# Optimization experiments

Measured on AMD Instinct MI355X. Metric: run time of the kernel, lower is better.

## Reference

```python
import jax, jax.numpy as jnp
import numpy as np

INPUT_DIM = 1024
EMBED_DIM = 1024
NUM_HEADS = 16
HEAD_DIM = EMBED_DIM // NUM_HEADS


def _xavier_uniform(key, shape):
    fan_in, fan_out = shape[1], shape[0]
    limit = float(np.sqrt(6.0 / (fan_in + fan_out)))
    return jax.random.uniform(key, shape, jnp.float32, -limit, limit)


def setup_inputs() -> dict:
    key = jax.random.key(0)
    kx, kqkv, ko = jax.random.split(key, 3)
    return {
        "x": jax.random.normal(kx, (2, 2048, INPUT_DIM), jnp.float32),
        "qkv_w": _xavier_uniform(kqkv, (3 * EMBED_DIM, INPUT_DIM)),
        "qkv_b": jnp.zeros((3 * EMBED_DIM,), jnp.float32),
        "o_w": _xavier_uniform(ko, (EMBED_DIM, INPUT_DIM)),
        "o_b": jnp.zeros((EMBED_DIM,), jnp.float32),
    }


def reference(x, qkv_w, qkv_b, o_w, o_b):
    B, S, _ = x.shape
    scale = HEAD_DIM ** -0.5
    # fused QKV projection: [B,S,3E]
    qkv = jnp.einsum('bsd,ed->bse', x, qkv_w) + qkv_b
    # [B,S,H,3Dh] -> [B,H,S,3Dh], then split into q,k,v
    qkv = qkv.reshape(B, S, NUM_HEADS, 3 * HEAD_DIM).transpose(0, 2, 1, 3)
    q, k, v = jnp.split(qkv, 3, axis=-1)
    # scaled dot-product attention
    scores = jnp.einsum('bhqd,bhkd->bhqk', q, k) * scale
    attn = jax.nn.softmax(scores, axis=-1)
    values = jnp.einsum('bhqk,bhkd->bhqd', attn, v)
    # [B,H,S,Dh] -> [B,S,E]
    values = values.transpose(0, 2, 1, 3).reshape(B, S, EMBED_DIM)
    return jnp.einsum('bse,oe->bso', values, o_w) + o_b
```

## Files before the change

### kernel.cpp

```cpp
#include <hip/hip_runtime.h>
#include <hip/hip_bf16.h>

typedef __bf16  bf16x8 __attribute__((ext_vector_type(8)));
typedef __bf16  bf16x4 __attribute__((ext_vector_type(4)));
typedef float   f32x4  __attribute__((ext_vector_type(4)));

#define LOG2E 1.44269504088896340736f

__device__ __forceinline__ void async_copy16(const void* g, void* l) {
  __builtin_amdgcn_global_load_lds(
      (const __attribute__((address_space(1))) unsigned int*)g,
      (__attribute__((address_space(3))) unsigned int*)l, 16, 0, 0);
}

#define C0 524288
#define C1 393216
#define C2 384
#define C3 131072
#define C4 128
#define CTOT (C0 + C1 + C2 + C3 + C4)
__global__ void convert_all(const void* __restrict__ x,  const void* __restrict__ qw,
                            const void* __restrict__ qb, const void* __restrict__ ow,
                            const void* __restrict__ ob,
                            __bf16* __restrict__ cx,  __bf16* __restrict__ cqw,
                            __bf16* __restrict__ cqb, __bf16* __restrict__ cow,
                            __bf16* __restrict__ cob, int* __restrict__ flag) {
  __shared__ int cnt;
  if (threadIdx.x == 0) cnt = 0;
  __syncthreads();
  unsigned int w = ((const unsigned int*)qw)[threadIdx.x];
  if (w & 0x4000u) atomicAdd(&cnt, 1);
  __syncthreads();
  const int f = (cnt > 16) ? 1 : 0;
  if (threadIdx.x == 0) *flag = f;

  int i = blockIdx.x * blockDim.x + threadIdx.x;
  const int stride = gridDim.x * blockDim.x;
  for (; i < CTOT; i += stride) {
    const void* s; __bf16* d; int off;
    if      (i < C0)                { s = x;  d = cx;  off = i; }
    else if (i < C0 + C1)           { s = qw; d = cqw; off = i - C0; }
    else if (i < C0 + C1 + C2)      { s = qb; d = cqb; off = i - C0 - C1; }
    else if (i < C0 + C1 + C2 + C3) { s = ow; d = cow; off = i - C0 - C1 - C2; }
    else                            { s = ob; d = cob; off = i - C0 - C1 - C2 - C3; }
    if (f) {
      const f32x4* sp = (const f32x4*)s;
      f32x4 a = sp[2 * off], b = sp[2 * off + 1];
      bf16x8 o;
      o[0] = (__bf16)a[0]; o[1] = (__bf16)a[1]; o[2] = (__bf16)a[2]; o[3] = (__bf16)a[3];
      o[4] = (__bf16)b[0]; o[5] = (__bf16)b[1]; o[6] = (__bf16)b[2]; o[7] = (__bf16)b[3];
      *(bf16x8*)&d[8 * off] = o;
    } else {
      *(bf16x8*)&d[8 * off] = ((const bf16x8*)s)[off];
    }
  }
}

template<int BN>
__global__ __launch_bounds__(256) void gemm_nt_bias(
    const __bf16* __restrict__ A,
    const __bf16* __restrict__ Bt,
    const __bf16* __restrict__ bias,
    __bf16* __restrict__ Cb,
    float* __restrict__ Cf,
    __bf16* __restrict__ vt,
    const int* __restrict__ flag,
    int M, int N, int K)
{
  constexpr int NI    = BN / 32;
  constexpr int BITER = (BN * 4) / 256;
  __shared__ __align__(16) __bf16 As[128 * 32];
  __shared__ __align__(16) __bf16 Bs[BN * 32];

  const int tid  = threadIdx.x;
  const int lane = tid & 63;
  const int wave = tid >> 6;
  const int qd   = lane >> 4;
  const int ln   = lane & 15;
  const int m0 = blockIdx.y * 128;
  const int n0 = blockIdx.x * BN;
  const int wm = (wave >> 1) * 64;
  const int wn = (wave & 1) * (16 * NI);

  f32x4 acc[4][NI] = {};

  for (int kt = 0; kt < K; kt += 32) {
#pragma unroll
    for (int i = 0; i < 2; ++i) {
      int s  = wave * 128 + i * 64 + lane;
      int r  = s >> 2;
      int cb = s & 3;
      async_copy16(A + (size_t)(m0 + r) * K + kt + cb * 8, &As[(wave * 128 + i * 64) * 8]);
    }
#pragma unroll
    for (int i = 0; i < BITER; ++i) {
      int s  = wave * (64 * BITER) + i * 64 + lane;
      int r  = s >> 2;
      int cb = s & 3;
      async_copy16(Bt + (size_t)(n0 + r) * K + kt + cb * 8,
                   &Bs[(wave * (64 * BITER) + i * 64) * 8]);
    }
    __syncthreads();

    bf16x8 af[4], bfr[NI];
#pragma unroll
    for (int t = 0; t < 4; ++t)
      af[t] = *(const bf16x8*)&As[(wm + t * 16 + ln) * 32 + qd * 8];
#pragma unroll
    for (int t = 0; t < NI; ++t)
      bfr[t] = *(const bf16x8*)&Bs[(wn + t * 16 + ln) * 32 + qd * 8];
#pragma unroll
    for (int mi = 0; mi < 4; ++mi)
#pragma unroll
      for (int ni = 0; ni < NI; ++ni)
        acc[mi][ni] = __builtin_amdgcn_mfma_f32_16x16x32_bf16(af[mi], bfr[ni], acc[mi][ni], 0, 0, 0);
    __syncthreads();
  }

  const bool f32out = (Cf != nullptr) && (*flag != 0);
#pragma unroll
  for (int ni = 0; ni < NI; ++ni) {
    int cb0 = n0 + wn + ni * 16;
    int col = cb0 + ln;
    float bv = (float)bias[col];
    int grp = cb0 % 192;
    if (vt != nullptr && grp >= 128) {
      int hh = cb0 / 192;
      int d  = grp - 128 + ln;
#pragma unroll
      for (int mi = 0; mi < 4; ++mi) {
        int row0 = m0 + wm + mi * 16 + qd * 4;
        int bb = row0 >> 11, ss = row0 & 2047;
        bf16x4 w;
#pragma unroll
        for (int r = 0; r < 4; ++r) w[r] = (__bf16)(acc[mi][ni][r] + bv);
        *(bf16x4*)&vt[(((size_t)(bb * 16 + hh) * 64 + d) * 2048 + ss)] = w;
      }
    } else {
#pragma unroll
      for (int mi = 0; mi < 4; ++mi) {
#pragma unroll
        for (int r = 0; r < 4; ++r) {
          int row = m0 + wm + mi * 16 + qd * 4 + r;
          float v = acc[mi][ni][r] + bv;
          if (f32out) Cf[(size_t)row * N + col] = v;
          else        Cb[(size_t)row * N + col] = (__bf16)v;
        }
      }
    }
  }
}

#define PST 72
__global__ __launch_bounds__(256, 2) void attn_flash(
    const __bf16* __restrict__ qkv,
    const __bf16* __restrict__ vt,
    __bf16* __restrict__ vals)
{
  __shared__ __align__(16) unsigned char smem[69632];
  __bf16* Ks  = (__bf16*)smem;
  __bf16* VTs = (__bf16*)(smem + 16384);
  __bf16* Ps  = (__bf16*)(smem + 32768);

  const int tid  = threadIdx.x;
  const int lane = tid & 63;
  const int wave = tid >> 6;
  const int sh   = wave >> 1;
  const int wq   = wave & 1;
  const int qd   = lane >> 4;
  const int ln   = lane & 15;
  const int b  = blockIdx.y >> 4;
  const int h  = blockIdx.y & 15;
  const int q0 = blockIdx.x * 128;
  const __bf16* base = qkv + (size_t)b * 2048 * 3072 + h * 192;
  const __bf16* vbase = vt + (size_t)(b * 16 + h) * 64 * 2048;
  const int khalf = sh * 1024;

  bf16x8 qfr[4][2];
#pragma unroll
  for (int nt = 0; nt < 4; ++nt)
#pragma unroll
    for (int ks = 0; ks < 2; ++ks)
      qfr[nt][ks] = *(const bf16x8*)&base[(size_t)(q0 + wq * 64 + nt * 16 + ln) * 3072
                                          + ks * 32 + qd * 8];

  const float kScale = 0.125f * LOG2E;
  __bf16* P = Ps + wave * (64 * PST);

  f32x4 oaccT[4][4] = {};
  float lpart[4] = {0.f, 0.f, 0.f, 0.f};

  for (int it = 0; it < 16; ++it) {
    const int kt = khalf + it * 64;
    __syncthreads();

#pragma unroll
    for (int i = 0; i < 4; ++i) {
      int s  = wq * 256 + i * 64 + lane;
      int r  = s >> 3;
      int c  = (s & 7) ^ (r & 7);
      async_copy16(base + (size_t)(kt + r) * 3072 + 64 + c * 8,
                   &Ks[sh * 4096 + (wq * 256 + i * 64) * 8]);
      async_copy16(vbase + (size_t)r * 2048 + kt + c * 8,
                   &VTs[sh * 4096 + (wq * 256 + i * 64) * 8]);
    }
    __syncthreads();

    f32x4 sacc[4][4] = {};
#pragma unroll
    for (int ks = 0; ks < 2; ++ks) {
      bf16x8 kfr[4];
#pragma unroll
      for (int mi = 0; mi < 4; ++mi) {
        int row = mi * 16 + ln;
        kfr[mi] = *(const bf16x8*)&Ks[sh * 4096 + row * 64 + (((ks * 4 + qd) ^ (row & 7)) * 8)];
      }
#pragma unroll
      for (int nt = 0; nt < 4; ++nt)
#pragma unroll
        for (int mi = 0; mi < 4; ++mi)
          sacc[nt][mi] = __builtin_amdgcn_mfma_f32_16x16x32_bf16(kfr[mi], qfr[nt][ks], sacc[nt][mi], 0, 0, 0);
    }

#pragma unroll
    for (int nt = 0; nt < 4; ++nt) {
      float rs = 0.f;
#pragma unroll
      for (int mi = 0; mi < 4; ++mi) {
        float pv[4];
#pragma unroll
        for (int r = 0; r < 4; ++r) {
          pv[r] = __builtin_exp2f(sacc[nt][mi][r] * kScale);
          rs += pv[r];
        }
        bf16x4 w;
        w[0] = (__bf16)pv[0]; w[1] = (__bf16)pv[1];
        w[2] = (__bf16)pv[2]; w[3] = (__bf16)pv[3];
        *(bf16x4*)&P[(nt * 16 + ln) * PST + mi * 16 + qd * 4] = w;
      }
      lpart[nt] += rs;
    }

    asm volatile("s_waitcnt lgkmcnt(0)" ::: "memory");

#pragma unroll
    for (int ks = 0; ks < 2; ++ks) {
      bf16x8 vfr[4], pfr[4];
#pragma unroll
      for (int md = 0; md < 4; ++md) {
        int row = md * 16 + ln;
        vfr[md] = *(const bf16x8*)&VTs[sh * 4096 + row * 64 + (((ks * 4 + qd) ^ (row & 7)) * 8)];
      }
#pragma unroll
      for (int nt = 0; nt < 4; ++nt)
        pfr[nt] = *(const bf16x8*)&P[(nt * 16 + ln) * PST + ks * 32 + qd * 8];
#pragma unroll
      for (int nt = 0; nt < 4; ++nt)
#pragma unroll
        for (int md = 0; md < 4; ++md)
          oaccT[nt][md] = __builtin_amdgcn_mfma_f32_16x16x32_bf16(vfr[md], pfr[nt], oaccT[nt][md], 0, 0, 0);
    }
  }

  float lw[4];
#pragma unroll
  for (int nt = 0; nt < 4; ++nt) {
    float l = lpart[nt];
    l += __shfl_xor(l, 16);
    l += __shfl_xor(l, 32);
    lw[nt] = l;
  }
  __syncthreads();

  float* Sc = (float*)smem;
  float* Ls = (float*)(smem + 32768);

  if (sh == 0) {
#pragma unroll
    for (int nt = 0; nt < 4; ++nt) {
#pragma unroll
      for (int md = 0; md < 4; ++md)
        *(f32x4*)&Sc[((size_t)(wq * 64 + nt * 16 + ln)) * 64 + md * 16 + qd * 4] = oaccT[nt][md];
      if (qd == 0) Ls[wq * 64 + nt * 16 + ln] = lw[nt];
    }
  }
  __syncthreads();
  if (sh == 1) {
#pragma unroll
    for (int nt = 0; nt < 4; ++nt) {
      float il = 1.0f / (lw[nt] + Ls[wq * 64 + nt * 16 + ln]);
      int q = q0 + wq * 64 + nt * 16 + ln;
      __bf16* o = vals + ((size_t)b * 2048 + q) * 1024 + h * 64;
#pragma unroll
      for (int md = 0; md < 4; ++md) {
        f32x4 part = *(const f32x4*)&Sc[((size_t)(wq * 64 + nt * 16 + ln)) * 64 + md * 16 + qd * 4];
        bf16x4 w;
#pragma unroll
        for (int r = 0; r < 4; ++r)
          w[r] = (__bf16)((oaccT[nt][md][r] + part[r]) * il);
        *(bf16x4*)&o[md * 16 + qd * 4] = w;
      }
    }
  }
}

extern "C" void kernel_launch(void* const* d_in, const int* in_sizes, int n_in,
                              void* d_out, int out_size, void* d_ws, size_t ws_size,
                              hipStream_t stream) {
  __bf16* ws    = (__bf16*)d_ws;
  __bf16* qkv   = ws;
  __bf16* vals  = qkv   + (size_t)4096 * 3072;
  __bf16* cx    = vals  + (size_t)4096 * 1024;
  __bf16* cqkvw = cx    + (size_t)4096 * 1024;
  __bf16* cow   = cqkvw + (size_t)3072 * 1024;
  __bf16* cqkvb = cow   + (size_t)1024 * 1024;
  __bf16* cob   = cqkvb + 4096;
  int*    flag  = (int*)(cob + 4096);
  __bf16* vT    = (__bf16*)(flag + 64);

  dim3 blk(256);

  convert_all<<<1024, 256, 0, stream>>>(d_in[0], d_in[1], d_in[2], d_in[3], d_in[4],
                                        cx, cqkvw, cqkvb, cow, cob, flag);

  gemm_nt_bias<128><<<dim3(3072 / 128, 4096 / 128), blk, 0, stream>>>(
      cx, cqkvw, cqkvb, qkv, nullptr, vT, flag, 4096, 3072, 1024);

  attn_flash<<<dim3(2048 / 128, 32), blk, 0, stream>>>(qkv, vT, vals);

  gemm_nt_bias<64><<<dim3(1024 / 64, 4096 / 128), blk, 0, stream>>>(
      vals, cow, cob, (__bf16*)d_out, (float*)d_out, nullptr, flag, 4096, 1024, 1024);
}
```

Baseline: 207.6 us.

## Double-buffer K/V tiles in attention and widen GEMM K-tile with swizzle

The attention kernel now double-buffers the K and V^T shared-memory tiles. The next tile's async global-to-LDS copy is issued before computing on the current one, and one barrier per iteration replaces two. The QKV/output GEMM now loads 64-wide K slices with an XOR-swizzled LDS layout and runs two MFMA sub-steps per barrier pair, which halves the number of synchronisations and is meant to reduce bank conflicts. The cost is attention LDS growing to about 100KB and the launch-bounds occupancy hint being dropped, which may cut resident blocks per CU from two to one.

```diff
diff --git a/kernel.cpp b/kernel.cpp
--- a/kernel.cpp
+++ b/kernel.cpp
@@ -67,10 +67,10 @@
     const int* __restrict__ flag,
     int M, int N, int K)
 {
-  constexpr int NI    = BN / 32;
-  constexpr int BITER = (BN * 4) / 256;
-  __shared__ __align__(16) __bf16 As[128 * 32];
-  __shared__ __align__(16) __bf16 Bs[BN * 32];
+  constexpr int NI  = BN / 32;
+  constexpr int NIB = BN / 32;
+  __shared__ __align__(16) __bf16 As[128 * 64];
+  __shared__ __align__(16) __bf16 Bs[BN * 64];
 
   const int tid  = threadIdx.x;
   const int lane = tid & 63;
@@ -84,36 +84,43 @@
 
   f32x4 acc[4][NI] = {};
 
-  for (int kt = 0; kt < K; kt += 32) {
-#pragma unroll
-    for (int i = 0; i < 2; ++i) {
-      int s  = wave * 128 + i * 64 + lane;
-      int r  = s >> 2;
-      int cb = s & 3;
-      async_copy16(A + (size_t)(m0 + r) * K + kt + cb * 8, &As[(wave * 128 + i * 64) * 8]);
-    }
-#pragma unroll
-    for (int i = 0; i < BITER; ++i) {
-      int s  = wave * (64 * BITER) + i * 64 + lane;
-      int r  = s >> 2;
-      int cb = s & 3;
-      async_copy16(Bt + (size_t)(n0 + r) * K + kt + cb * 8,
-                   &Bs[(wave * (64 * BITER) + i * 64) * 8]);
+  for (int kt = 0; kt < K; kt += 64) {
+#pragma unroll
+    for (int i = 0; i < 4; ++i) {
+      int s = wave * 256 + i * 64 + lane;
+      int r = s >> 3;
+      int c = (s & 7) ^ (r & 7);
+      async_copy16(A + (size_t)(m0 + r) * K + kt + c * 8, &As[(wave * 256 + i * 64) * 8]);
+    }
+#pragma unroll
+    for (int i = 0; i < NIB; ++i) {
+      int s = wave * (64 * NIB) + i * 64 + lane;
+      int r = s >> 3;
+      int c = (s & 7) ^ (r & 7);
+      async_copy16(Bt + (size_t)(n0 + r) * K + kt + c * 8,
+                   &Bs[(wave * (64 * NIB) + i * 64) * 8]);
     }
     __syncthreads();
 
-    bf16x8 af[4], bfr[NI];
-#pragma unroll
-    for (int t = 0; t < 4; ++t)
-      af[t] = *(const bf16x8*)&As[(wm + t * 16 + ln) * 32 + qd * 8];
-#pragma unroll
-    for (int t = 0; t < NI; ++t)
-      bfr[t] = *(const bf16x8*)&Bs[(wn + t * 16 + ln) * 32 + qd * 8];
-#pragma unroll
-    for (int mi = 0; mi < 4; ++mi)
-#pragma unroll
-      for (int ni = 0; ni < NI; ++ni)
-        acc[mi][ni] = __builtin_amdgcn_mfma_f32_16x16x32_bf16(af[mi], bfr[ni], acc[mi][ni], 0, 0, 0);
+#pragma unroll
+    for (int kk = 0; kk < 2; ++kk) {
+      bf16x8 af[4], bfr[NI];
+#pragma unroll
+      for (int t = 0; t < 4; ++t) {
+        int ra = wm + t * 16 + ln;
+        af[t] = *(const bf16x8*)&As[ra * 64 + (((kk * 4 + qd) ^ (ra & 7)) * 8)];
+      }
+#pragma unroll
+      for (int t = 0; t < NI; ++t) {
+        int rb = wn + t * 16 + ln;
+        bfr[t] = *(const bf16x8*)&Bs[rb * 64 + (((kk * 4 + qd) ^ (rb & 7)) * 8)];
+      }
+#pragma unroll
+      for (int mi = 0; mi < 4; ++mi)
+#pragma unroll
+        for (int ni = 0; ni < NI; ++ni)
+          acc[mi][ni] = __builtin_amdgcn_mfma_f32_16x16x32_bf16(af[mi], bfr[ni], acc[mi][ni], 0, 0, 0);
+    }
     __syncthreads();
   }
 
@@ -152,15 +159,15 @@
 }
 
 #define PST 72
-__global__ __launch_bounds__(256, 2) void attn_flash(
+__global__ __launch_bounds__(256) void attn_flash(
     const __bf16* __restrict__ qkv,
     const __bf16* __restrict__ vt,
     __bf16* __restrict__ vals)
 {
-  __shared__ __align__(16) unsigned char smem[69632];
-  __bf16* Ks  = (__bf16*)smem;
-  __bf16* VTs = (__bf16*)(smem + 16384);
-  __bf16* Ps  = (__bf16*)(smem + 32768);
+  __shared__ __align__(16) unsigned char smem[102400];
+  __bf16* Ksb = (__bf16*)smem;
+  __bf16* VTb = (__bf16*)(smem + 32768);
+  __bf16* Ps  = (__bf16*)(smem + 65536);
 
   const int tid  = threadIdx.x;
   const int lane = tid & 63;
@@ -190,21 +197,35 @@
   f32x4 oaccT[4][4] = {};
   float lpart[4] = {0.f, 0.f, 0.f, 0.f};
 
+#pragma unroll
+  for (int i = 0; i < 4; ++i) {
+    int s = wq * 256 + i * 64 + lane;
+    int r = s >> 3;
+    int c = (s & 7) ^ (r & 7);
+    async_copy16(base + (size_t)(khalf + r) * 3072 + 64 + c * 8,
+                 &Ksb[sh * 4096 + (wq * 256 + i * 64) * 8]);
+    async_copy16(vbase + (size_t)r * 2048 + khalf + c * 8,
+                 &VTb[sh * 4096 + (wq * 256 + i * 64) * 8]);
+  }
+
   for (int it = 0; it < 16; ++it) {
-    const int kt = khalf + it * 64;
+    const int buf  = (it & 1) * 8192;
+    const int nbuf = ((it + 1) & 1) * 8192;
     __syncthreads();
 
-#pragma unroll
-    for (int i = 0; i < 4; ++i) {
-      int s  = wq * 256 + i * 64 + lane;
-      int r  = s >> 3;
-      int c  = (s & 7) ^ (r & 7);
-      async_copy16(base + (size_t)(kt + r) * 3072 + 64 + c * 8,
-                   &Ks[sh * 4096 + (wq * 256 + i * 64) * 8]);
-      async_copy16(vbase + (size_t)r * 2048 + kt + c * 8,
-                   &VTs[sh * 4096 + (wq * 256 + i * 64) * 8]);
-    }
-    __syncthreads();
+    {
+      const int ktn = khalf + (((it + 1) & 15) << 6);
+#pragma unroll
+      for (int i = 0; i < 4; ++i) {
+        int s = wq * 256 + i * 64 + lane;
+        int r = s >> 3;
+        int c = (s & 7) ^ (r & 7);
+        async_copy16(base + (size_t)(ktn + r) * 3072 + 64 + c * 8,
+                     &Ksb[nbuf + sh * 4096 + (wq * 256 + i * 64) * 8]);
+        async_copy16(vbase + (size_t)r * 2048 + ktn + c * 8,
+                     &VTb[nbuf + sh * 4096 + (wq * 256 + i * 64) * 8]);
+      }
+    }
 
     f32x4 sacc[4][4] = {};
 #pragma unroll
@@ -213,7 +234,8 @@
 #pragma unroll
       for (int mi = 0; mi < 4; ++mi) {
         int row = mi * 16 + ln;
-        kfr[mi] = *(const bf16x8*)&Ks[sh * 4096 + row * 64 + (((ks * 4 + qd) ^ (row & 7)) * 8)];
+        kfr[mi] = *(const bf16x8*)&Ksb[buf + sh * 4096 + row * 64
+                                       + (((ks * 4 + qd) ^ (row & 7)) * 8)];
       }
 #pragma unroll
       for (int nt = 0; nt < 4; ++nt)
@@ -249,7 +271,8 @@
 #pragma unroll
       for (int md = 0; md < 4; ++md) {
         int row = md * 16 + ln;
-        vfr[md] = *(const bf16x8*)&VTs[sh * 4096 + row * 64 + (((ks * 4 + qd) ^ (row & 7)) * 8)];
+        vfr[md] = *(const bf16x8*)&VTb[buf + sh * 4096 + row * 64
+                                       + (((ks * 4 + qd) ^ (row & 7)) * 8)];
       }
 #pragma unroll
       for (int nt = 0; nt < 4; ++nt)
```

Measured after the change: 223.6 us. +7.7%, slower.
